# Performance work log

Hardware: AMD Instinct MI355X
Metric: run time of the kernel (lower is better)

Reference implementation:

```python
import jax, jax.numpy as jnp
import numpy as np

B, N_NODES, VOCAB, H = 128, 1023, 2048, 256  # depth-9 perfect binary trees (heap layout)


def setup_inputs() -> dict:
    key = jax.random.key(0)
    k1, k2, k3, k4, k5 = jax.random.split(key, 5)
    tokens = jax.random.randint(k1, (B, N_NODES), 0, VOCAB)
    emb = jax.random.normal(k2, (VOCAB, H), dtype=jnp.float32) * 0.02
    Wx = jax.random.normal(k3, (H, 5 * H), dtype=jnp.float32) * 0.02
    Ul = jax.random.normal(k4, (H, 5 * H), dtype=jnp.float32) * 0.02
    Ur = jax.random.normal(k5, (H, 5 * H), dtype=jnp.float32) * 0.02
    b = jnp.zeros((5 * H,), dtype=jnp.float32)
    return {"tokens": tokens, "emb": emb, "Wx": Wx, "Ul": Ul, "Ur": Ur, "b": b}


def _tree_lstm(tokens, emb, Wx, Ul, Ur, b):
    # tokens: [B, 2^(D+1)-1] in level-order heap layout; children of heap index i
    # are 2i+1, 2i+2 -> within level d+1 they sit at offsets 2k, 2k+1.
    n_nodes = tokens.shape[1]
    depth = int(np.log2(n_nodes + 1)) - 1
    hdim = emb.shape[1]
    x_all = emb[tokens]  # [B, N, H] embedding lookup (memory-bound gather)
    h = c = None
    for d in range(depth, -1, -1):  # bottom-up over levels (fixed structural loop)
        start, n = 2 ** d - 1, 2 ** d
        x = x_all[:, start:start + n]  # [B, n, H]
        gates = jnp.einsum('bnh,hg->bng', x, Wx) + b
        if h is not None:
            hl, hr = h[:, 0::2], h[:, 1::2]
            cl, cr = c[:, 0::2], c[:, 1::2]
            gates = gates + jnp.einsum('bnh,hg->bng', hl, Ul) + jnp.einsum('bnh,hg->bng', hr, Ur)
        i, fl, fr, o, u = jnp.split(gates, 5, axis=-1)
        i, fl, fr, o = map(jax.nn.sigmoid, (i, fl, fr, o))
        u = jnp.tanh(u)
        c_new = i * u
        if c is not None:
            c_new = c_new + fl * cl + fr * cr
        c = c_new
        h = o * jnp.tanh(c)
    return h[:, 0], c[:, 0]  # root states, each [B, H]


def reference(tokens, emb, Wx, Ul, Ur, b):
    h_root, _ = _tree_lstm(tokens, emb, Wx, Ul, Ur, b)
    return h_root  # [B, H]
```

## Files before the change

kernel.cpp:

```cpp
#include <hip/hip_runtime.h>
#include <hip/hip_bf16.h>
#include <math.h>

#define B_SZ   128
#define HDIM   256
#define NG     1280
#define NNODES 1023
#define VOCAB  2048

typedef unsigned int uint32;
typedef short  short8v  __attribute__((ext_vector_type(8)));
typedef float  float4v  __attribute__((ext_vector_type(4)));

__device__ __forceinline__ float sigm(float x) {
    return 1.0f / (1.0f + __expf(-x));
}
__device__ __forceinline__ float tanh_fast(float x) {
    return 2.0f / (1.0f + __expf(-2.0f * x)) - 1.0f;
}
__device__ __forceinline__ float bf2f(unsigned short u) {
    return __uint_as_float(((uint32)u) << 16);
}
__device__ __forceinline__ unsigned short f2bf(float f) {
    uint32 x = __float_as_uint(f);
    uint32 r = (x + 0x7FFFu + ((x >> 16) & 1u)) >> 16;
    return (unsigned short)r;
}

__device__ __forceinline__ void dma16(const unsigned short* gptr, unsigned short* lptr) {
    __builtin_amdgcn_global_load_lds(
        (const __attribute__((address_space(1))) void*)gptr,
        (__attribute__((address_space(3))) void*)lptr, 16, 0, 0);
}

__global__ __launch_bounds__(256) void ew_kernel(
    const float* __restrict__ emb, const float* __restrict__ Wx,
    const float* __restrict__ bias, unsigned short* __restrict__ EWb)
{
    __shared__ float As[16][76];
    __shared__ float Bs[16][72];

    const int tid = threadIdx.x;
    const int tx = tid & 15, ty = tid >> 4;
    const int rowBase = blockIdx.x * 64;
    const int colBase = blockIdx.y * 64;

    const int a_rr = tid >> 2, a_kq = tid & 3;
    const int b_kk = tid >> 4, b_c4 = tid & 15;

    float acc[4][4] = {};

    for (int kb = 0; kb < 256; kb += 16) {
        float4 av = *(const float4*)(emb + (size_t)(rowBase + a_rr) * 256 + kb + a_kq * 4);
        float4 bv = *(const float4*)(Wx + (size_t)(kb + b_kk) * NG + colBase + b_c4 * 4);
        __syncthreads();
        As[a_kq * 4 + 0][a_rr] = av.x;
        As[a_kq * 4 + 1][a_rr] = av.y;
        As[a_kq * 4 + 2][a_rr] = av.z;
        As[a_kq * 4 + 3][a_rr] = av.w;
        *(float4*)&Bs[b_kk][b_c4 * 4] = bv;
        __syncthreads();
        #pragma unroll
        for (int k = 0; k < 16; ++k) {
            float4 a = *(const float4*)&As[k][ty * 4];
            float4 b = *(const float4*)&Bs[k][tx * 4];
            acc[0][0] += a.x * b.x; acc[0][1] += a.x * b.y; acc[0][2] += a.x * b.z; acc[0][3] += a.x * b.w;
            acc[1][0] += a.y * b.x; acc[1][1] += a.y * b.y; acc[1][2] += a.y * b.z; acc[1][3] += a.y * b.w;
            acc[2][0] += a.z * b.x; acc[2][1] += a.z * b.y; acc[2][2] += a.z * b.z; acc[2][3] += a.z * b.w;
            acc[3][0] += a.w * b.x; acc[3][1] += a.w * b.y; acc[3][2] += a.w * b.z; acc[3][3] += a.w * b.w;
        }
    }

    #pragma unroll
    for (int u = 0; u < 4; ++u) {
        const int row = rowBase + ty * 4 + u;
        const int col = colBase + tx * 4;
        float4 bb = *(const float4*)(bias + col);
        ushort4 ov;
        ov.x = f2bf(acc[u][0] + bb.x);
        ov.y = f2bf(acc[u][1] + bb.y);
        ov.z = f2bf(acc[u][2] + bb.z);
        ov.w = f2bf(acc[u][3] + bb.w);
        *(ushort4*)(EWb + (size_t)row * NG + col) = ov;
    }
}

__global__ __launch_bounds__(256) void embb_kernel(
    const float* __restrict__ emb, unsigned short* __restrict__ embb)
{
    const int t = blockIdx.x * 256 + threadIdx.x;
    const float4 v0 = *(const float4*)(emb + (size_t)t * 8);
    const float4 v1 = *(const float4*)(emb + (size_t)t * 8 + 4);
    short8v o;
    o[0] = (short)f2bf(v0.x); o[1] = (short)f2bf(v0.y);
    o[2] = (short)f2bf(v0.z); o[3] = (short)f2bf(v0.w);
    o[4] = (short)f2bf(v1.x); o[5] = (short)f2bf(v1.y);
    o[6] = (short)f2bf(v1.z); o[7] = (short)f2bf(v1.w);
    *(short8v*)(embb + (size_t)t * 8) = o;
}

__global__ __launch_bounds__(256) void prep_wtf(
    const float* __restrict__ Ul, const float* __restrict__ Ur,
    const float* __restrict__ Wx, unsigned short* __restrict__ WTf)
{
    const int t = blockIdx.x * 256 + threadIdx.x;
    const int l = t & 63;
    const int q = l >> 4, c = l & 15;
    const int ks = (t >> 6) % 24;
    const int ng = t / (24 * 64);
    const int col = ng * 16 + c;
    const int k = ks * 32 + q * 8;
    const float* src = (k < 256) ? (Ul + (size_t)k * NG + col)
                     : (k < 512) ? (Ur + (size_t)(k - 256) * NG + col)
                                 : (Wx + (size_t)(k - 512) * NG + col);
    short8v v;
    #pragma unroll
    for (int j = 0; j < 8; ++j) v[j] = (short)f2bf(src[(size_t)j * NG]);
    *(short8v*)(WTf + (size_t)t * 8) = v;
}

__global__ __launch_bounds__(256, 2) void leaf_kernel(
    const unsigned short* __restrict__ WTf, const unsigned short* __restrict__ embb,
    const float* __restrict__ bias, const int* __restrict__ tokens,
    unsigned short* __restrict__ hdst, unsigned short* __restrict__ cdst)
{
    __shared__ __align__(16) unsigned short Ab[2][4096];
    __shared__ __align__(16) unsigned short wb[2 * 4096];

    const int tid  = threadIdx.x;
    const int lane = tid & 63;
    const int w    = tid >> 6;
    const int quad = lane >> 4, col15 = lane & 15;
    const int jt = blockIdx.x;
    const int rowBase = blockIdx.y * 64;
    const int jbase   = jt * 64;

    const unsigned short* agp[2];
    unsigned short* ldst[2];
    #pragma unroll
    for (int t = 0; t < 2; ++t) {
        const int ch = 2 * w + t, sub = ch >> 2, rt = ch & 3;
        const int srow = rowBase + rt * 16 + col15;
        const int sb = srow >> 9, si = srow & 511;
        const int stok = tokens[sb * NNODES + 511 + si];
        agp[t]  = embb + (size_t)stok * HDIM + sub * 32 + quad * 8;
        ldst[t] = &Ab[0][0] + ch * 512;
    }

    const short8v* WTfv = (const short8v*)WTf;
    uint32 boff[3];
    boff[0] = ((0 * 16 + jt * 4 + w) * 24 + 16) * 64 + lane;
    boff[1] = ((3 * 16 + jt * 4 + w) * 24 + 16) * 64 + lane;
    boff[2] = ((4 * 16 + jt * 4 + w) * 24 + 16) * 64 + lane;

    float4v acc[4][3];
    #pragma unroll
    for (int rt = 0; rt < 4; ++rt)
        #pragma unroll
        for (int gi = 0; gi < 3; ++gi)
            #pragma unroll
            for (int e = 0; e < 4; ++e) acc[rt][gi][e] = 0.0f;

    dma16(agp[0], ldst[0]); dma16(agp[1], ldst[1]);
    __syncthreads();

    #pragma unroll
    for (int s = 0; s < 4; ++s) {
        if (s < 3) {
            dma16(agp[0] + (s + 1) * 64, ldst[0] + ((s + 1) & 1) * 4096);
            dma16(agp[1] + (s + 1) * 64, ldst[1] + ((s + 1) & 1) * 4096);
        }
        #pragma unroll
        for (int sub = 0; sub < 2; ++sub) {
            short8v bf[3];
            #pragma unroll
            for (int gi = 0; gi < 3; ++gi) bf[gi] = WTfv[boff[gi] + (s * 2 + sub) * 64];
            #pragma unroll
            for (int rt = 0; rt < 4; ++rt) {
                const short8v af = *(const short8v*)&Ab[s & 1][(sub * 4 + rt) * 512 + lane * 8];
                #pragma unroll
                for (int gi = 0; gi < 3; ++gi)
                    acc[rt][gi] = __builtin_amdgcn_mfma_f32_16x16x32_bf16(
                        af, bf[gi], acc[rt][gi], 0, 0, 0);
            }
        }
        __syncthreads();
    }

    const int jl = w * 16 + col15;
    const int j  = jbase + jl;
    const float b_i = bias[j], b_o = bias[768 + j], b_u = bias[1024 + j];
    const int jchunk = jl >> 3, jpos = jl & 7;

    #pragma unroll
    for (int rt = 0; rt < 4; ++rt) {
        #pragma unroll
        for (int reg = 0; reg < 4; ++reg) {
            const int rr = rt * 16 + quad * 4 + reg;
            const float gi = acc[rt][0][reg] + b_i;
            const float go = acc[rt][1][reg] + b_o;
            const float gu = acc[rt][2][reg] + b_u;
            const float c = sigm(gi) * tanh_fast(gu);
            const float h = sigm(go) * tanh_fast(c);
            const int roff = ((jchunk + 2 * quad) & 7) * 8 + jpos;
            wb[rr * 64 + roff]        = f2bf(h);
            wb[4096 + rr * 64 + roff] = f2bf(c);
        }
    }
    __syncthreads();
    #pragma unroll
    for (int k2 = 0; k2 < 4; ++k2) {
        const int c = tid + k2 * 256;
        const int arr = c >> 9, rr = (c >> 3) & 63, u = c & 7;
        const int ru = (u + 2 * ((rr >> 2) & 3)) & 7;
        const short8v v = *(const short8v*)(wb + (arr * 4096 + rr * 64 + ru * 8));
        unsigned short* dstp = (arr ? cdst : hdst) +
            (size_t)(rowBase + rr) * HDIM + jbase + u * 8;
        *(short8v*)dstp = v;
    }
}

__global__ __launch_bounds__(256, 2) void level_kernel(
    const unsigned short* __restrict__ WTf, const unsigned short* __restrict__ EWb,
    const int* __restrict__ tokens,
    const unsigned short* __restrict__ hsrc, const unsigned short* __restrict__ csrc,
    unsigned short* __restrict__ hdst, unsigned short* __restrict__ cdst,
    float* __restrict__ out, const int d)
{
    const int n = 1 << d;

    __shared__ __align__(16) unsigned short Ab[2][4096];
    __shared__ __align__(16) unsigned short ews[2560 * 8];
    __shared__ __align__(16) unsigned short cst[1024 * 8];

    const int tid  = threadIdx.x;
    const int lane = tid & 63;
    const int w    = tid >> 6;
    const int quad = lane >> 4, col15 = lane & 15;
    const int jt = blockIdx.x;
    const int rowBase = blockIdx.y * 64;
    const int jbase   = jt * 64;

    const unsigned short* agp[2];
    unsigned short* ldst[2];
    #pragma unroll
    for (int t = 0; t < 2; ++t) {
        const int ch = 2 * w + t, sub = ch >> 2, rt = ch & 3;
        const int srow = rowBase + rt * 16 + col15;
        agp[t]  = hsrc + (size_t)(2 * srow) * HDIM + sub * 32 + quad * 8;
        ldst[t] = &Ab[0][0] + ch * 512;
    }

    const short8v* WTfv = (const short8v*)WTf;
    uint32 boff[5];
    #pragma unroll
    for (int g = 0; g < 5; ++g)
        boff[g] = ((g * 16 + jt * 4 + w) * 24) * 64 + lane;

    float4v acc[4][5];
    #pragma unroll
    for (int rt = 0; rt < 4; ++rt)
        #pragma unroll
        for (int g = 0; g < 5; ++g)
            #pragma unroll
            for (int e = 0; e < 4; ++e) acc[rt][g][e] = 0.0f;

    dma16(agp[0], ldst[0]); dma16(agp[1], ldst[1]);
    __syncthreads();

    #pragma unroll
    for (int s = 0; s < 8; ++s) {
        if (s < 7) {
            dma16(agp[0] + (s + 1) * 64, ldst[0] + ((s + 1) & 1) * 4096);
            dma16(agp[1] + (s + 1) * 64, ldst[1] + ((s + 1) & 1) * 4096);
        }

        if (s >= 2 && s <= 6) {
            #pragma unroll
            for (int t2 = 0; t2 < 2; ++t2) {
                const int it = (s - 2) * 2 + t2;
                const int c = tid + it * 256;
                const uint32 row = (uint32)c / 40u;
                const int rem = c - (int)row * 40;
                const int g = rem >> 3, u = rem & 7;
                const int grow = rowBase + (int)row;
                const int tok = tokens[(grow >> d) * NNODES + (n - 1) + (grow & (n - 1))];
                dma16(EWb + (size_t)tok * NG + g * 256 + jbase + u * 8,
                      ews + ((size_t)it * 256 + w * 64) * 8);
            }
            if (s >= 5) {
                #pragma unroll
                for (int t2 = 0; t2 < 2; ++t2) {
                    const int k2 = (s - 5) * 2 + t2;
                    const int c = tid + k2 * 256;
                    const int rr = c >> 4, side = (c >> 3) & 1, u = c & 7;
                    dma16(csrc + (size_t)(2 * (rowBase + rr) + side) * HDIM + jbase + u * 8,
                          cst + ((size_t)k2 * 256 + w * 64) * 8);
                }
            }
        }

        #pragma unroll
        for (int sub = 0; sub < 2; ++sub) {
            short8v bf[5];
            #pragma unroll
            for (int g = 0; g < 5; ++g) bf[g] = WTfv[boff[g] + (s * 2 + sub) * 64];
            #pragma unroll
            for (int rt = 0; rt < 4; ++rt) {
                const short8v af = *(const short8v*)&Ab[s & 1][(sub * 4 + rt) * 512 + lane * 8];
                #pragma unroll
                for (int g = 0; g < 5; ++g)
                    acc[rt][g] = __builtin_amdgcn_mfma_f32_16x16x32_bf16(
                        af, bf[g], acc[rt][g], 0, 0, 0);
            }
        }
        __syncthreads();
    }

    const int jl = w * 16 + col15;
    const int j  = jbase + jl;
    float hv[4][4], cv[4][4];
    #pragma unroll
    for (int rt = 0; rt < 4; ++rt) {
        #pragma unroll
        for (int reg = 0; reg < 4; ++reg) {
            const int rr = rt * 16 + quad * 4 + reg;
            const float gi  = acc[rt][0][reg] + bf2f(ews[rr * 320 +       jl]);
            const float gfl = acc[rt][1][reg] + bf2f(ews[rr * 320 +  64 + jl]);
            const float gfr = acc[rt][2][reg] + bf2f(ews[rr * 320 + 128 + jl]);
            const float go  = acc[rt][3][reg] + bf2f(ews[rr * 320 + 192 + jl]);
            const float gu  = acc[rt][4][reg] + bf2f(ews[rr * 320 + 256 + jl]);
            const float cl  = bf2f(cst[rr * 128 +      jl]);
            const float cr  = bf2f(cst[rr * 128 + 64 + jl]);
            const float ii = sigm(gi), fl = sigm(gfl), fr = sigm(gfr), oo = sigm(go);
            const float uu = tanh_fast(gu);
            const float c = ii * uu + fl * cl + fr * cr;
            const float h = oo * tanh_fast(c);
            cv[rt][reg] = c; hv[rt][reg] = h;
            if (d == 0) out[(size_t)(rowBase + rr) * HDIM + j] = h;
        }
    }
    __syncthreads();

    const int jchunk = jl >> 3, jpos = jl & 7;
    #pragma unroll
    for (int rt = 0; rt < 4; ++rt) {
        #pragma unroll
        for (int reg = 0; reg < 4; ++reg) {
            const int rr = rt * 16 + quad * 4 + reg;
            const int roff = ((jchunk + 2 * quad) & 7) * 8 + jpos;
            ews[rr * 64 + roff]        = f2bf(hv[rt][reg]);
            ews[4096 + rr * 64 + roff] = f2bf(cv[rt][reg]);
        }
    }
    __syncthreads();
    #pragma unroll
    for (int k2 = 0; k2 < 4; ++k2) {
        const int c = tid + k2 * 256;
        const int arr = c >> 9, rr = (c >> 3) & 63, u = c & 7;
        const int ru = (u + 2 * ((rr >> 2) & 3)) & 7;
        const short8v v = *(const short8v*)(ews + (arr * 4096 + rr * 64 + ru * 8));
        unsigned short* dstp = (arr ? cdst : hdst) +
            (size_t)(rowBase + rr) * HDIM + jbase + u * 8;
        *(short8v*)dstp = v;
    }
}

extern "C" void kernel_launch(void* const* d_in, const int* in_sizes, int n_in,
                              void* d_out, int out_size, void* d_ws, size_t ws_size,
                              hipStream_t stream)
{
    const int*   tokens = (const int*)d_in[0];
    const float* emb    = (const float*)d_in[1];
    const float* Wx     = (const float*)d_in[2];
    const float* Ul     = (const float*)d_in[3];
    const float* Ur     = (const float*)d_in[4];
    const float* bias   = (const float*)d_in[5];
    float* out = (float*)d_out;

    const size_t EW_ELEMS  = (size_t)VOCAB * NG;
    const size_t EMB_ELEMS = (size_t)VOCAB * HDIM;
    const size_t WTF_ELEMS = (size_t)80 * 24 * 64 * 8;
    const size_t SLOT_A    = (size_t)512 * B_SZ * HDIM;
    const size_t SLOT_B    = (size_t)256 * B_SZ * HDIM;
    const size_t REQUIRED  = (EW_ELEMS + EMB_ELEMS + WTF_ELEMS + 2 * (SLOT_A + SLOT_B)) * 2;
    if (ws_size < REQUIRED || d_ws == nullptr) return;

    char* ws = (char*)d_ws;
    unsigned short* EWb  = (unsigned short*)ws;
    unsigned short* embb = EWb + EW_ELEMS;
    unsigned short* WTf  = embb + EMB_ELEMS;
    unsigned short* hA   = WTf + WTF_ELEMS;
    unsigned short* cA   = hA + SLOT_A;
    unsigned short* hB   = cA + SLOT_A;
    unsigned short* cB   = hB + SLOT_B;

    ew_kernel<<<dim3(VOCAB / 64, NG / 64), 256, 0, stream>>>(emb, Wx, bias, EWb);
    embb_kernel<<<dim3(256), 256, 0, stream>>>(emb, embb);
    prep_wtf<<<dim3(480), 256, 0, stream>>>(Ul, Ur, Wx, WTf);

    leaf_kernel<<<dim3(4, 1024), 256, 0, stream>>>(WTf, embb, bias, tokens, hA, cA);

    for (int d = 8; d >= 0; --d) {
        const int NRB = 2 << d;
        const bool evenD = ((d & 1) == 0);
        const unsigned short* hs = evenD ? hA : hB;
        const unsigned short* cs = evenD ? cA : cB;
        unsigned short* hd = evenD ? hB : hA;
        unsigned short* cd = evenD ? cB : cA;
        level_kernel<<<dim3(4, NRB), 256, 0, stream>>>(
            WTf, EWb, tokens, hs, cs, hd, cd, out, d);
    }
}
```

Baseline: 385.3 us.

## Double row tile to 128 per block in leaf and level kernels

```diff
diff --git a/kernel.cpp b/kernel.cpp
--- a/kernel.cpp
+++ b/kernel.cpp
@@ -124,22 +124,22 @@
     const float* __restrict__ bias, const int* __restrict__ tokens,
     unsigned short* __restrict__ hdst, unsigned short* __restrict__ cdst)
 {
-    __shared__ __align__(16) unsigned short Ab[2][4096];
-    __shared__ __align__(16) unsigned short wb[2 * 4096];
+    __shared__ __align__(16) unsigned short Ab[2][8192];
+    __shared__ __align__(16) unsigned short wb[16384];
 
     const int tid  = threadIdx.x;
     const int lane = tid & 63;
     const int w    = tid >> 6;
     const int quad = lane >> 4, col15 = lane & 15;
     const int jt = blockIdx.x;
-    const int rowBase = blockIdx.y * 64;
+    const int rowBase = blockIdx.y * 128;
     const int jbase   = jt * 64;
 
-    const unsigned short* agp[2];
-    unsigned short* ldst[2];
-    #pragma unroll
-    for (int t = 0; t < 2; ++t) {
-        const int ch = 2 * w + t, sub = ch >> 2, rt = ch & 3;
+    const unsigned short* agp[4];
+    unsigned short* ldst[4];
+    #pragma unroll
+    for (int t = 0; t < 4; ++t) {
+        const int ch = 4 * w + t, sub = ch >> 3, rt = ch & 7;
         const int srow = rowBase + rt * 16 + col15;
         const int sb = srow >> 9, si = srow & 511;
         const int stok = tokens[sb * NNODES + 511 + si];
@@ -153,22 +153,24 @@
     boff[1] = ((3 * 16 + jt * 4 + w) * 24 + 16) * 64 + lane;
     boff[2] = ((4 * 16 + jt * 4 + w) * 24 + 16) * 64 + lane;
 
-    float4v acc[4][3];
-    #pragma unroll
-    for (int rt = 0; rt < 4; ++rt)
+    float4v acc[8][3];
+    #pragma unroll
+    for (int rt = 0; rt < 8; ++rt)
         #pragma unroll
         for (int gi = 0; gi < 3; ++gi)
             #pragma unroll
             for (int e = 0; e < 4; ++e) acc[rt][gi][e] = 0.0f;
 
-    dma16(agp[0], ldst[0]); dma16(agp[1], ldst[1]);
+    #pragma unroll
+    for (int t = 0; t < 4; ++t) dma16(agp[t], ldst[t]);
     __syncthreads();
 
     #pragma unroll
     for (int s = 0; s < 4; ++s) {
         if (s < 3) {
-            dma16(agp[0] + (s + 1) * 64, ldst[0] + ((s + 1) & 1) * 4096);
-            dma16(agp[1] + (s + 1) * 64, ldst[1] + ((s + 1) & 1) * 4096);
+            #pragma unroll
+            for (int t = 0; t < 4; ++t)
+                dma16(agp[t] + (s + 1) * 64, ldst[t] + ((s + 1) & 1) * 8192);
         }
         #pragma unroll
         for (int sub = 0; sub < 2; ++sub) {
@@ -176,8 +178,8 @@
             #pragma unroll
             for (int gi = 0; gi < 3; ++gi) bf[gi] = WTfv[boff[gi] + (s * 2 + sub) * 64];
             #pragma unroll
-            for (int rt = 0; rt < 4; ++rt) {
-                const short8v af = *(const short8v*)&Ab[s & 1][(sub * 4 + rt) * 512 + lane * 8];
+            for (int rt = 0; rt < 8; ++rt) {
+                const short8v af = *(const short8v*)&Ab[s & 1][(sub * 8 + rt) * 512 + lane * 8];
                 #pragma unroll
                 for (int gi = 0; gi < 3; ++gi)
                     acc[rt][gi] = __builtin_amdgcn_mfma_f32_16x16x32_bf16(
@@ -193,7 +195,7 @@
     const int jchunk = jl >> 3, jpos = jl & 7;
 
     #pragma unroll
-    for (int rt = 0; rt < 4; ++rt) {
+    for (int rt = 0; rt < 8; ++rt) {
         #pragma unroll
         for (int reg = 0; reg < 4; ++reg) {
             const int rr = rt * 16 + quad * 4 + reg;
@@ -204,23 +206,23 @@
             const float h = sigm(go) * tanh_fast(c);
             const int roff = ((jchunk + 2 * quad) & 7) * 8 + jpos;
             wb[rr * 64 + roff]        = f2bf(h);
-            wb[4096 + rr * 64 + roff] = f2bf(c);
+            wb[8192 + rr * 64 + roff] = f2bf(c);
         }
     }
     __syncthreads();
     #pragma unroll
-    for (int k2 = 0; k2 < 4; ++k2) {
+    for (int k2 = 0; k2 < 8; ++k2) {
         const int c = tid + k2 * 256;
-        const int arr = c >> 9, rr = (c >> 3) & 63, u = c & 7;
+        const int arr = c >> 10, rr = (c >> 3) & 127, u = c & 7;
         const int ru = (u + 2 * ((rr >> 2) & 3)) & 7;
-        const short8v v = *(const short8v*)(wb + (arr * 4096 + rr * 64 + ru * 8));
+        const short8v v = *(const short8v*)(wb + (arr * 8192 + rr * 64 + ru * 8));
         unsigned short* dstp = (arr ? cdst : hdst) +
             (size_t)(rowBase + rr) * HDIM + jbase + u * 8;
         *(short8v*)dstp = v;
     }
 }
 
-__global__ __launch_bounds__(256, 2) void level_kernel(
+__global__ __launch_bounds__(256, 1) void level_kernel(
     const unsigned short* __restrict__ WTf, const unsigned short* __restrict__ EWb,
     const int* __restrict__ tokens,
     const unsigned short* __restrict__ hsrc, const unsigned short* __restrict__ csrc,
@@ -229,23 +231,23 @@
 {
     const int n = 1 << d;
 
-    __shared__ __align__(16) unsigned short Ab[2][4096];
-    __shared__ __align__(16) unsigned short ews[2560 * 8];
-    __shared__ __align__(16) unsigned short cst[1024 * 8];
+    __shared__ __align__(16) unsigned short Ab[2][8192];
+    __shared__ __align__(16) unsigned short ews[40960];
+    __shared__ __align__(16) unsigned short cst[16384];
 
     const int tid  = threadIdx.x;
     const int lane = tid & 63;
     const int w    = tid >> 6;
     const int quad = lane >> 4, col15 = lane & 15;
     const int jt = blockIdx.x;
-    const int rowBase = blockIdx.y * 64;
+    const int rowBase = blockIdx.y * 128;
     const int jbase   = jt * 64;
 
-    const unsigned short* agp[2];
-    unsigned short* ldst[2];
-    #pragma unroll
-    for (int t = 0; t < 2; ++t) {
-        const int ch = 2 * w + t, sub = ch >> 2, rt = ch & 3;
+    const unsigned short* agp[4];
+    unsigned short* ldst[4];
+    #pragma unroll
+    for (int t = 0; t < 4; ++t) {
+        const int ch = 4 * w + t, sub = ch >> 3, rt = ch & 7;
         const int srow = rowBase + rt * 16 + col15;
         agp[t]  = hsrc + (size_t)(2 * srow) * HDIM + sub * 32 + quad * 8;
         ldst[t] = &Ab[0][0] + ch * 512;
@@ -257,43 +259,48 @@
     for (int g = 0; g < 5; ++g)
         boff[g] = ((g * 16 + jt * 4 + w) * 24) * 64 + lane;
 
-    float4v acc[4][5];
-    #pragma unroll
-    for (int rt = 0; rt < 4; ++rt)
+    float4v acc[8][5];
+    #pragma unroll
+    for (int rt = 0; rt < 8; ++rt)
         #pragma unroll
         for (int g = 0; g < 5; ++g)
             #pragma unroll
             for (int e = 0; e < 4; ++e) acc[rt][g][e] = 0.0f;
 
-    dma16(agp[0], ldst[0]); dma16(agp[1], ldst[1]);
+    #pragma unroll
+    for (int t = 0; t < 4; ++t) dma16(agp[t], ldst[t]);
     __syncthreads();
 
     #pragma unroll
     for (int s = 0; s < 8; ++s) {
         if (s < 7) {
-            dma16(agp[0] + (s + 1) * 64, ldst[0] + ((s + 1) & 1) * 4096);
-            dma16(agp[1] + (s + 1) * 64, ldst[1] + ((s + 1) & 1) * 4096);
+            #pragma unroll
+            for (int t = 0; t < 4; ++t)
+                dma16(agp[t] + (s + 1) * 64, ldst[t] + ((s + 1) & 1) * 8192);
         }
 
         if (s >= 2 && s <= 6) {
             #pragma unroll
-            for (int t2 = 0; t2 < 2; ++t2) {
-                const int it = (s - 2) * 2 + t2;
+            for (int t2 = 0; t2 < 4; ++t2) {
+                const int it = (s - 2) * 4 + t2;
                 const int c = tid + it * 256;
-                const uint32 row = (uint32)c / 40u;
-                const int rem = c - (int)row * 40;
-                const int g = rem >> 3, u = rem & 7;
-                const int grow = rowBase + (int)row;
+                const uint32 rr = (uint32)c / 40u;
+                const int rem = c - (int)rr * 40;
+                const int g = rem >> 3, su = rem & 7;
+                const int u = su ^ (((int)rr >> 2) & 7);
+                const int grow = rowBase + (int)rr;
                 const int tok = tokens[(grow >> d) * NNODES + (n - 1) + (grow & (n - 1))];
                 dma16(EWb + (size_t)tok * NG + g * 256 + jbase + u * 8,
                       ews + ((size_t)it * 256 + w * 64) * 8);
             }
             if (s >= 5) {
                 #pragma unroll
-                for (int t2 = 0; t2 < 2; ++t2) {
-                    const int k2 = (s - 5) * 2 + t2;
+                for (int t2 = 0; t2 < 4; ++t2) {
+                    const int k2 = (s - 5) * 4 + t2;
                     const int c = tid + k2 * 256;
-                    const int rr = c >> 4, side = (c >> 3) & 1, u = c & 7;
+                    const int rr = c >> 4, rem = c & 15;
+                    const int side = rem >> 3, su = rem & 7;
+                    const int u = su ^ ((rr >> 2) & 7);
                     dma16(csrc + (size_t)(2 * (rowBase + rr) + side) * HDIM + jbase + u * 8,
                           cst + ((size_t)k2 * 256 + w * 64) * 8);
                 }
@@ -306,8 +313,8 @@
             #pragma unroll
             for (int g = 0; g < 5; ++g) bf[g] = WTfv[boff[g] + (s * 2 + sub) * 64];
             #pragma unroll
-            for (int rt = 0; rt < 4; ++rt) {
-                const short8v af = *(const short8v*)&Ab[s & 1][(sub * 4 + rt) * 512 + lane * 8];
+            for (int rt = 0; rt < 8; ++rt) {
+                const short8v af = *(const short8v*)&Ab[s & 1][(sub * 8 + rt) * 512 + lane * 8];
                 #pragma unroll
                 for (int g = 0; g < 5; ++g)
                     acc[rt][g] = __builtin_amdgcn_mfma_f32_16x16x32_bf16(
@@ -317,49 +324,43 @@
         __syncthreads();
     }
 
+    unsigned short* const wb = &Ab[0][0];
     const int jl = w * 16 + col15;
     const int j  = jbase + jl;
-    float hv[4][4], cv[4][4];
-    #pragma unroll
-    for (int rt = 0; rt < 4; ++rt) {
+    const int uu8 = jl >> 3, pos = jl & 7;
+    #pragma unroll
+    for (int rt = 0; rt < 8; ++rt) {
+        const int xr = (rt * 4 + quad) & 7;
+        const int eb = ((rt * 16 + quad * 4) * 40 + (uu8 ^ xr)) * 8 + pos;
+        const int cb = ((rt * 16 + quad * 4) * 16 + (uu8 ^ xr)) * 8 + pos;
         #pragma unroll
         for (int reg = 0; reg < 4; ++reg) {
             const int rr = rt * 16 + quad * 4 + reg;
-            const float gi  = acc[rt][0][reg] + bf2f(ews[rr * 320 +       jl]);
-            const float gfl = acc[rt][1][reg] + bf2f(ews[rr * 320 +  64 + jl]);
-            const float gfr = acc[rt][2][reg] + bf2f(ews[rr * 320 + 128 + jl]);
-            const float go  = acc[rt][3][reg] + bf2f(ews[rr * 320 + 192 + jl]);
-            const float gu  = acc[rt][4][reg] + bf2f(ews[rr * 320 + 256 + jl]);
-            const float cl  = bf2f(cst[rr * 128 +      jl]);
-            const float cr  = bf2f(cst[rr * 128 + 64 + jl]);
+            const float gi  = acc[rt][0][reg] + bf2f(ews[eb + reg * 320]);
+            const float gfl = acc[rt][1][reg] + bf2f(ews[eb + reg * 320 + 64]);
+            const float gfr = acc[rt][2][reg] + bf2f(ews[eb + reg * 320 + 128]);
+            const float go  = acc[rt][3][reg] + bf2f(ews[eb + reg * 320 + 192]);
+            const float gu  = acc[rt][4][reg] + bf2f(ews[eb + reg * 320 + 256]);
+            const float cl  = bf2f(cst[cb + reg * 128]);
+            const float cr  = bf2f(cst[cb + reg * 128 + 64]);
             const float ii = sigm(gi), fl = sigm(gfl), fr = sigm(gfr), oo = sigm(go);
             const float uu = tanh_fast(gu);
             const float c = ii * uu + fl * cl + fr * cr;
             const float h = oo * tanh_fast(c);
-            cv[rt][reg] = c; hv[rt][reg] = h;
+            const int roff = ((uu8 + 2 * quad) & 7) * 8 + pos;
+            wb[rr * 64 + roff]        = f2bf(h);
+            wb[8192 + rr * 64 + roff] = f2bf(c);
             if (d == 0) out[(size_t)(rowBase + rr) * HDIM + j] = h;
         }
     }
     __syncthreads();
 
-    const int jchunk = jl >> 3, jpos = jl & 7;
-    #pragma unroll
-    for (int rt = 0; rt < 4; ++rt) {
-        #pragma unroll
-        for (int reg = 0; reg < 4; ++reg) {
-            const int rr = rt * 16 + quad * 4 + reg;
-            const int roff = ((jchunk + 2 * quad) & 7) * 8 + jpos;
-            ews[rr * 64 + roff]        = f2bf(hv[rt][reg]);
-            ews[4096 + rr * 64 + roff] = f2bf(cv[rt][reg]);
-        }
-    }
-    __syncthreads();
-    #pragma unroll
-    for (int k2 = 0; k2 < 4; ++k2) {
+    #pragma unroll
+    for (int k2 = 0; k2 < 8; ++k2) {
         const int c = tid + k2 * 256;
-        const int arr = c >> 9, rr = (c >> 3) & 63, u = c & 7;
+        const int arr = c >> 10, rr = (c >> 3) & 127, u = c & 7;
         const int ru = (u + 2 * ((rr >> 2) & 3)) & 7;
-        const short8v v = *(const short8v*)(ews + (arr * 4096 + rr * 64 + ru * 8));
+        const short8v v = *(const short8v*)(wb + (arr * 8192 + rr * 64 + ru * 8));
         unsigned short* dstp = (arr ? cdst : hdst) +
             (size_t)(rowBase + rr) * HDIM + jbase + u * 8;
         *(short8v*)dstp = v;
@@ -399,10 +400,10 @@
     embb_kernel<<<dim3(256), 256, 0, stream>>>(emb, embb);
     prep_wtf<<<dim3(480), 256, 0, stream>>>(Ul, Ur, Wx, WTf);
 
-    leaf_kernel<<<dim3(4, 1024), 256, 0, stream>>>(WTf, embb, bias, tokens, hA, cA);
+    leaf_kernel<<<dim3(4, 512), 256, 0, stream>>>(WTf, embb, bias, tokens, hA, cA);
 
     for (int d = 8; d >= 0; --d) {
-        const int NRB = 2 << d;
+        const int NRB = 1 << d;
         const bool evenD = ((d & 1) == 0);
         const unsigned short* hs = evenD ? hA : hB;
         const unsigned short* cs = evenD ? cA : cB;
```

New measurement: 526.4 us. +36.6%, slower.

## Cut LDS footprint, double-buffer B fragments, and split level epilogue into halves

Applied to the files above, without the earlier changes.

```diff
diff --git a/kernel.cpp b/kernel.cpp
--- a/kernel.cpp
+++ b/kernel.cpp
@@ -119,13 +119,12 @@
     *(short8v*)(WTf + (size_t)t * 8) = v;
 }
 
-__global__ __launch_bounds__(256, 2) void leaf_kernel(
+__global__ __launch_bounds__(256, 4) void leaf_kernel(
     const unsigned short* __restrict__ WTf, const unsigned short* __restrict__ embb,
     const float* __restrict__ bias, const int* __restrict__ tokens,
     unsigned short* __restrict__ hdst, unsigned short* __restrict__ cdst)
 {
     __shared__ __align__(16) unsigned short Ab[2][4096];
-    __shared__ __align__(16) unsigned short wb[2 * 4096];
 
     const int tid  = threadIdx.x;
     const int lane = tid & 63;
@@ -161,6 +160,10 @@
             #pragma unroll
             for (int e = 0; e < 4; ++e) acc[rt][gi][e] = 0.0f;
 
+    short8v bbuf[2][3];
+    #pragma unroll
+    for (int gi = 0; gi < 3; ++gi) bbuf[0][gi] = WTfv[boff[gi]];
+
     dma16(agp[0], ldst[0]); dma16(agp[1], ldst[1]);
     __syncthreads();
 
@@ -172,21 +175,25 @@
         }
         #pragma unroll
         for (int sub = 0; sub < 2; ++sub) {
-            short8v bf[3];
-            #pragma unroll
-            for (int gi = 0; gi < 3; ++gi) bf[gi] = WTfv[boff[gi] + (s * 2 + sub) * 64];
+            const int ks = s * 2 + sub;
+            if (ks < 7) {
+                #pragma unroll
+                for (int gi = 0; gi < 3; ++gi)
+                    bbuf[(ks + 1) & 1][gi] = WTfv[boff[gi] + (size_t)(ks + 1) * 64];
+            }
             #pragma unroll
             for (int rt = 0; rt < 4; ++rt) {
                 const short8v af = *(const short8v*)&Ab[s & 1][(sub * 4 + rt) * 512 + lane * 8];
                 #pragma unroll
                 for (int gi = 0; gi < 3; ++gi)
                     acc[rt][gi] = __builtin_amdgcn_mfma_f32_16x16x32_bf16(
-                        af, bf[gi], acc[rt][gi], 0, 0, 0);
+                        af, bbuf[ks & 1][gi], acc[rt][gi], 0, 0, 0);
             }
         }
         __syncthreads();
     }
 
+    unsigned short* const wb = &Ab[0][0];
     const int jl = w * 16 + col15;
     const int j  = jbase + jl;
     const float b_i = bias[j], b_o = bias[768 + j], b_u = bias[1024 + j];
@@ -220,7 +227,7 @@
     }
 }
 
-__global__ __launch_bounds__(256, 2) void level_kernel(
+__global__ __launch_bounds__(256, 3) void level_kernel(
     const unsigned short* __restrict__ WTf, const unsigned short* __restrict__ EWb,
     const int* __restrict__ tokens,
     const unsigned short* __restrict__ hsrc, const unsigned short* __restrict__ csrc,
@@ -230,8 +237,8 @@
     const int n = 1 << d;
 
     __shared__ __align__(16) unsigned short Ab[2][4096];
-    __shared__ __align__(16) unsigned short ews[2560 * 8];
-    __shared__ __align__(16) unsigned short cst[1024 * 8];
+    __shared__ __align__(16) unsigned short ews[10240];
+    __shared__ __align__(16) unsigned short cst[4096];
 
     const int tid  = threadIdx.x;
     const int lane = tid & 63;
@@ -265,6 +272,10 @@
             #pragma unroll
             for (int e = 0; e < 4; ++e) acc[rt][g][e] = 0.0f;
 
+    short8v bbuf[2][5];
+    #pragma unroll
+    for (int g = 0; g < 5; ++g) bbuf[0][g] = WTfv[boff[g]];
+
     dma16(agp[0], ldst[0]); dma16(agp[1], ldst[1]);
     __syncthreads();
 
@@ -274,95 +285,116 @@
             dma16(agp[0] + (s + 1) * 64, ldst[0] + ((s + 1) & 1) * 4096);
             dma16(agp[1] + (s + 1) * 64, ldst[1] + ((s + 1) & 1) * 4096);
         }
-
         if (s >= 2 && s <= 6) {
-            #pragma unroll
-            for (int t2 = 0; t2 < 2; ++t2) {
-                const int it = (s - 2) * 2 + t2;
-                const int c = tid + it * 256;
-                const uint32 row = (uint32)c / 40u;
-                const int rem = c - (int)row * 40;
-                const int g = rem >> 3, u = rem & 7;
-                const int grow = rowBase + (int)row;
-                const int tok = tokens[(grow >> d) * NNODES + (n - 1) + (grow & (n - 1))];
-                dma16(EWb + (size_t)tok * NG + g * 256 + jbase + u * 8,
-                      ews + ((size_t)it * 256 + w * 64) * 8);
-            }
-            if (s >= 5) {
+            const int it = s - 2;
+            const int c = tid + it * 256;
+            const uint32 rl = (uint32)c / 40u;
+            const int rem = c - (int)rl * 40;
+            const int g = rem >> 3, su = rem & 7;
+            const int u = su ^ (((int)rl >> 2) & 7);
+            const int grow = rowBase + (int)rl;
+            const int tok = tokens[(grow >> d) * NNODES + (n - 1) + (grow & (n - 1))];
+            dma16(EWb + (size_t)tok * NG + g * 256 + jbase + u * 8,
+                  ews + ((size_t)it * 256 + w * 64) * 8);
+        }
+        if (s >= 6) {
+            const int it = s - 6;
+            const int c = tid + it * 256;
+            const int rl = c >> 4, side = (c >> 3) & 1, su = c & 7;
+            const int u = su ^ ((rl >> 2) & 7);
+            dma16(csrc + (size_t)(2 * (rowBase + rl) + side) * HDIM + jbase + u * 8,
+                  cst + ((size_t)it * 256 + w * 64) * 8);
+        }
+
+        #pragma unroll
+        for (int sub = 0; sub < 2; ++sub) {
+            const int ks = s * 2 + sub;
+            if (ks < 15) {
                 #pragma unroll
-                for (int t2 = 0; t2 < 2; ++t2) {
-                    const int k2 = (s - 5) * 2 + t2;
-                    const int c = tid + k2 * 256;
-                    const int rr = c >> 4, side = (c >> 3) & 1, u = c & 7;
-                    dma16(csrc + (size_t)(2 * (rowBase + rr) + side) * HDIM + jbase + u * 8,
-                          cst + ((size_t)k2 * 256 + w * 64) * 8);
-                }
-            }
-        }
-
-        #pragma unroll
-        for (int sub = 0; sub < 2; ++sub) {
-            short8v bf[5];
-            #pragma unroll
-            for (int g = 0; g < 5; ++g) bf[g] = WTfv[boff[g] + (s * 2 + sub) * 64];
+                for (int g = 0; g < 5; ++g)
+                    bbuf[(ks + 1) & 1][g] = WTfv[boff[g] + (size_t)(ks + 1) * 64];
+            }
             #pragma unroll
             for (int rt = 0; rt < 4; ++rt) {
                 const short8v af = *(const short8v*)&Ab[s & 1][(sub * 4 + rt) * 512 + lane * 8];
                 #pragma unroll
                 for (int g = 0; g < 5; ++g)
                     acc[rt][g] = __builtin_amdgcn_mfma_f32_16x16x32_bf16(
-                        af, bf[g], acc[rt][g], 0, 0, 0);
+                        af, bbuf[ks & 1][g], acc[rt][g], 0, 0, 0);
             }
         }
         __syncthreads();
     }
 
+    unsigned short* const wb = &Ab[0][0];
     const int jl = w * 16 + col15;
     const int j  = jbase + jl;
-    float hv[4][4], cv[4][4];
-    #pragma unroll
-    for (int rt = 0; rt < 4; ++rt) {
-        #pragma unroll
-        for (int reg = 0; reg < 4; ++reg) {
-            const int rr = rt * 16 + quad * 4 + reg;
-            const float gi  = acc[rt][0][reg] + bf2f(ews[rr * 320 +       jl]);
-            const float gfl = acc[rt][1][reg] + bf2f(ews[rr * 320 +  64 + jl]);
-            const float gfr = acc[rt][2][reg] + bf2f(ews[rr * 320 + 128 + jl]);
-            const float go  = acc[rt][3][reg] + bf2f(ews[rr * 320 + 192 + jl]);
-            const float gu  = acc[rt][4][reg] + bf2f(ews[rr * 320 + 256 + jl]);
-            const float cl  = bf2f(cst[rr * 128 +      jl]);
-            const float cr  = bf2f(cst[rr * 128 + 64 + jl]);
-            const float ii = sigm(gi), fl = sigm(gfl), fr = sigm(gfr), oo = sigm(go);
-            const float uu = tanh_fast(gu);
-            const float c = ii * uu + fl * cl + fr * cr;
-            const float h = oo * tanh_fast(c);
-            cv[rt][reg] = c; hv[rt][reg] = h;
-            if (d == 0) out[(size_t)(rowBase + rr) * HDIM + j] = h;
-        }
-    }
-    __syncthreads();
-
-    const int jchunk = jl >> 3, jpos = jl & 7;
-    #pragma unroll
-    for (int rt = 0; rt < 4; ++rt) {
-        #pragma unroll
-        for (int reg = 0; reg < 4; ++reg) {
-            const int rr = rt * 16 + quad * 4 + reg;
-            const int roff = ((jchunk + 2 * quad) & 7) * 8 + jpos;
-            ews[rr * 64 + roff]        = f2bf(hv[rt][reg]);
-            ews[4096 + rr * 64 + roff] = f2bf(cv[rt][reg]);
-        }
-    }
-    __syncthreads();
-    #pragma unroll
-    for (int k2 = 0; k2 < 4; ++k2) {
-        const int c = tid + k2 * 256;
-        const int arr = c >> 9, rr = (c >> 3) & 63, u = c & 7;
-        const int ru = (u + 2 * ((rr >> 2) & 3)) & 7;
-        const short8v v = *(const short8v*)(ews + (arr * 4096 + rr * 64 + ru * 8));
-        unsigned short* dstp = (arr ? cdst : hdst) +
-            (size_t)(rowBase + rr) * HDIM + jbase + u * 8;
-        *(short8v*)dstp = v;
+    const int uu8 = jl >> 3, pos = jl & 7;
+
+    #pragma unroll
+    for (int p = 0; p < 2; ++p) {
+        #pragma unroll
+        for (int rt2 = 0; rt2 < 2; ++rt2) {
+            const int rt = 2 * p + rt2;
+            const int rlb = rt2 * 16 + quad * 4;
+            const int xr = (rlb >> 2) & 7;
+            const int eb = rlb * 320 + (uu8 ^ xr) * 8 + pos;
+            const int cb = rlb * 128 + (uu8 ^ xr) * 8 + pos;
+            const int rb = rlb * 64 + ((uu8 + 2 * quad) & 7) * 8 + pos;
+            #pragma unroll
+            for (int reg = 0; reg < 4; ++reg) {
+                const float gi  = acc[rt][0][reg] + bf2f(ews[eb + reg * 320]);
+                const float gfl = acc[rt][1][reg] + bf2f(ews[eb + reg * 320 + 64]);
+                const float gfr = acc[rt][2][reg] + bf2f(ews[eb + reg * 320 + 128]);
+                const float go  = acc[rt][3][reg] + bf2f(ews[eb + reg * 320 + 192]);
+                const float gu  = acc[rt][4][reg] + bf2f(ews[eb + reg * 320 + 256]);
+                const float cl  = bf2f(cst[cb + reg * 128]);
+                const float cr  = bf2f(cst[cb + reg * 128 + 64]);
+                const float ii = sigm(gi), fl = sigm(gfl), fr = sigm(gfr), oo = sigm(go);
+                const float uu = tanh_fast(gu);
+                const float c = ii * uu + fl * cl + fr * cr;
+                const float h = oo * tanh_fast(c);
+                wb[rb + reg * 64]        = f2bf(h);
+                wb[2048 + rb + reg * 64] = f2bf(c);
+                if (d == 0) out[(size_t)(rowBase + rt * 16 + quad * 4 + reg) * HDIM + j] = h;
+            }
+        }
+        __syncthreads();
+
+        if (p == 0) {
+            #pragma unroll
+            for (int it = 0; it < 5; ++it) {
+                const int c = tid + it * 256;
+                const uint32 rl = (uint32)c / 40u;
+                const int rem = c - (int)rl * 40;
+                const int g = rem >> 3, su = rem & 7;
+                const int u = su ^ (((int)rl >> 2) & 7);
+                const int grow = rowBase + 32 + (int)rl;
+                const int tok = tokens[(grow >> d) * NNODES + (n - 1) + (grow & (n - 1))];
+                dma16(EWb + (size_t)tok * NG + g * 256 + jbase + u * 8,
+                      ews + ((size_t)it * 256 + w * 64) * 8);
+            }
+            #pragma unroll
+            for (int it = 0; it < 2; ++it) {
+                const int c = tid + it * 256;
+                const int rl = c >> 4, side = (c >> 3) & 1, su = c & 7;
+                const int u = su ^ ((rl >> 2) & 7);
+                dma16(csrc + (size_t)(2 * (rowBase + 32 + rl) + side) * HDIM + jbase + u * 8,
+                      cst + ((size_t)it * 256 + w * 64) * 8);
+            }
+        }
+
+        #pragma unroll
+        for (int k2 = 0; k2 < 2; ++k2) {
+            const int c = tid + k2 * 256;
+            const int arr = c >> 8, rl = (c >> 3) & 31, u = c & 7;
+            const int ru = (u + 2 * ((rl >> 2) & 3)) & 7;
+            const short8v v = *(const short8v*)(wb + (arr * 2048 + rl * 64 + ru * 8));
+            unsigned short* dstp = (arr ? cdst : hdst) +
+                (size_t)(rowBase + 32 * p + rl) * HDIM + jbase + u * 8;
+            *(short8v*)dstp = v;
+        }
+        if (p == 0) __syncthreads();
     }
 }
 
```

Measured after the change: 412.3 us. 1.07x slower.
